# Performance work log

Hardware: AMD Instinct MI355X
Metric: run time of the kernel (lower is better)

## Reference

```python
import jax, jax.numpy as jnp
import numpy as np

N_RBF = 16
N_HIDDEN = 64
CUTOFF = 5.0
N_ATOMS = 4096


def setup_inputs() -> dict:
    key = jax.random.key(0)
    ks = jax.random.split(key, 7)
    # Scale positions so the 5.0 cutoff yields a sparse-ish neighbor graph.
    positions = jax.random.normal(ks[0], (N_ATOMS, 3), dtype=jnp.float32) * 10.0
    s1 = 1.0 / np.sqrt(N_RBF)
    s2 = 1.0 / np.sqrt(N_HIDDEN)
    W1 = jax.random.normal(ks[1], (N_RBF, N_HIDDEN), dtype=jnp.float32) * s1
    b1 = jax.random.normal(ks[2], (N_HIDDEN,), dtype=jnp.float32) * 0.01
    W2 = jax.random.normal(ks[3], (N_HIDDEN, N_HIDDEN), dtype=jnp.float32) * s2
    b2 = jax.random.normal(ks[4], (N_HIDDEN,), dtype=jnp.float32) * 0.01
    W3 = jax.random.normal(ks[5], (N_HIDDEN, 1), dtype=jnp.float32) * s2
    b3 = jax.random.normal(ks[6], (1,), dtype=jnp.float32) * 0.01
    return {"positions": positions, "W1": W1, "b1": b1, "W2": W2, "b2": b2, "W3": W3, "b3": b3}


def _features(positions):
    # positions: (N, 3) -> per-node RBF-aggregated features (N, n_rbf).
    # Equivalent to torch mask.nonzero + scatter_add: features[i] = sum_j in-cutoff rbf(d_ij).
    diff = positions[:, None, :] - positions[None, :, :]          # (N, N, 3)
    dist = jnp.sqrt(jnp.sum(diff * diff, axis=-1))                # (N, N)
    mask = (dist > 1e-6) & (dist < CUTOFF)                        # (N, N)
    centers = jnp.linspace(0.5, CUTOFF, N_RBF, dtype=jnp.float32) # (n_rbf,)
    eta = 0.5 * CUTOFF / N_RBF
    gauss = jnp.exp(-((dist[..., None] - centers) ** 2) / (2.0 * eta * eta))  # (N, N, n_rbf)
    x = jnp.minimum(dist / CUTOFF, 1.0)
    smooth = 0.5 * (1.0 + jnp.cos(jnp.float32(np.pi) * x))        # (N, N)
    w = jnp.where(mask, smooth, 0.0)                              # masked smooth-cutoff weight
    return jnp.einsum('ij,ijk->ik', w, gauss)                     # (N, n_rbf)


def reference(positions, W1, b1, W2, b2, W3, b3):
    feats = _features(positions)                                  # (N, n_rbf)
    h = jax.nn.silu(feats @ W1 + b1)
    h = jax.nn.silu(h @ W2 + b2)
    energy = jnp.sum(h @ W3 + b3)                                 # scalar
    return energy
```

## Files before the change

kernel.cpp:

```cpp
#include <hip/hip_runtime.h>

#define N_ATOMS  4096
#define N_RBF    16
#define N_HIDDEN 64
#define NTHREADS 1024
#define WPB      16
#define APB      8
#define NBLOCKS  (N_ATOMS / APB)
#define QCAP     192
#define HALF_J   (N_ATOMS / 2)

__global__ void zero_out_kernel(float* __restrict__ out) {
    if (threadIdx.x == 0 && blockIdx.x == 0) out[0] = 0.0f;
}

__device__ __forceinline__ void accum_rbf(float d2, float (&f)[N_RBF]) {
    const float d  = sqrtf(d2);
    const float sm = 0.5f + 0.5f * __cosf(0.62831853071795865f * d);
    #pragma unroll
    for (int k = 0; k < N_RBF; ++k) {
        const float t = d - (0.5f + 0.3f * (float)k);
        f[k] += sm * __expf(-20.48f * t * t);
    }
}

__device__ __forceinline__ int wave_prefix(unsigned long long m) {
    return __builtin_amdgcn_mbcnt_hi((unsigned)(m >> 32),
            __builtin_amdgcn_mbcnt_lo((unsigned)m, 0u));
}

__global__ __launch_bounds__(NTHREADS, 8) void fused_sr_kernel(
    const float* __restrict__ pos,
    const float* __restrict__ W1,
    const float* __restrict__ b1,
    const float* __restrict__ W2,
    const float* __restrict__ b2,
    const float* __restrict__ W3,
    const float* __restrict__ b3,
    float* __restrict__ out)
{
    __shared__ __align__(16) float4 sp[N_ATOMS];
    __shared__ __align__(16) float qd[WPB][QCAP];
    __shared__ float pairbuf[APB][2][N_RBF];
    __shared__ float ered[APB];

    const int tid = threadIdx.x;

    for (int idx = tid; idx < N_ATOMS; idx += NTHREADS) {
        sp[idx] = make_float4(pos[idx * 3 + 0], pos[idx * 3 + 1], pos[idx * 3 + 2], 0.0f);
    }
    __syncthreads();

    const int lane = tid & 63;
    const int wib  = tid >> 6;
    const int pid  = wib >> 1;
    const int half = wib & 1;
    const int i    = blockIdx.x * APB + pid;

    const float4 pi4 = sp[i];
    const float xi = pi4.x, yi = pi4.y, zi = pi4.z;

    int cnt = 0;
    const int jbase = half * HALF_J;
    #pragma unroll 4
    for (int j0 = 0; j0 < HALF_J; j0 += 64) {
        const float4 pj = sp[jbase + j0 + lane];
        const float dx = xi - pj.x;
        const float dy = yi - pj.y;
        const float dz = zi - pj.z;
        const float d2 = fmaf(dx, dx, fmaf(dy, dy, dz * dz));
        const bool act = (d2 < 25.0f) && (d2 > 1e-12f);
        const unsigned long long m = __ballot(act);
        int widx = cnt + wave_prefix(m);
        widx = widx < QCAP ? widx : QCAP - 1;
        if (act) qd[wib][widx] = d2;
        cnt += (int)__popcll(m);
    }

    float f[N_RBF];
    #pragma unroll
    for (int k = 0; k < N_RBF; ++k) f[k] = 0.0f;
    for (int b = 0; b < cnt; b += 64) {
        const int q = b + lane;
        accum_rbf((q < cnt) ? qd[wib][q] : 1e8f, f);
    }

    #pragma unroll
    for (int k = 0; k < N_RBF; ++k) {
        #pragma unroll
        for (int off = 32; off > 0; off >>= 1)
            f[k] += __shfl_xor(f[k], off, 64);
    }

    if (lane == 0) {
        #pragma unroll
        for (int k = 0; k < N_RBF; ++k) pairbuf[pid][half][k] = f[k];
    }
    __syncthreads();

    if (half == 0) {
        float a1 = b1[lane];
        #pragma unroll
        for (int k = 0; k < N_RBF; ++k)
            a1 = fmaf(f[k] + pairbuf[pid][1][k], W1[k * N_HIDDEN + lane], a1);
        const float h1 = a1 / (1.0f + __expf(-a1));

        float* h1p = &qd[pid][0];
        h1p[lane] = h1;
        float a2 = b2[lane];
        #pragma unroll
        for (int k = 0; k < N_HIDDEN; k += 4) {
            const float4 hv = *reinterpret_cast<const float4*>(&h1p[k]);
            a2 = fmaf(hv.x, W2[(k + 0) * N_HIDDEN + lane], a2);
            a2 = fmaf(hv.y, W2[(k + 1) * N_HIDDEN + lane], a2);
            a2 = fmaf(hv.z, W2[(k + 2) * N_HIDDEN + lane], a2);
            a2 = fmaf(hv.w, W2[(k + 3) * N_HIDDEN + lane], a2);
        }
        const float h2 = a2 / (1.0f + __expf(-a2));

        float e = h2 * W3[lane];
        #pragma unroll
        for (int off = 32; off > 0; off >>= 1)
            e += __shfl_xor(e, off, 64);
        if (lane == 0) ered[pid] = e;
    }
    __syncthreads();
    if (tid == 0) {
        float acc = 0.0f;
        #pragma unroll
        for (int w = 0; w < APB; ++w) acc += ered[w];
        atomicAdd(out, acc + (float)APB * b3[0]);
    }
}

extern "C" void kernel_launch(void* const* d_in, const int* in_sizes, int n_in,
                              void* d_out, int out_size, void* d_ws, size_t ws_size,
                              hipStream_t stream) {
    const float* pos = (const float*)d_in[0];
    const float* W1  = (const float*)d_in[1];
    const float* b1  = (const float*)d_in[2];
    const float* W2  = (const float*)d_in[3];
    const float* b2  = (const float*)d_in[4];
    const float* W3  = (const float*)d_in[5];
    const float* b3  = (const float*)d_in[6];
    float* out = (float*)d_out;

    zero_out_kernel<<<1, 64, 0, stream>>>(out);
    fused_sr_kernel<<<NBLOCKS, NTHREADS, 0, stream>>>(pos, W1, b1, W2, b2, W3, b3, out);
}
```

Measured before the change: 86.29 us.

## Process two atoms per wave in neighbor scan and rebalance RBF/MLP across waves

Each block now handles 16 atoms instead of 8, and each wave scans half the j range for two atoms at once, so every loaded neighbor position is reused for two distance tests. After the scan, the per-wave queues are regrouped so that each wave owns one atom. That wave runs the RBF accumulation and the MLP for its atom, using a shared-memory transpose to finish the feature reduction. This halves the number of blocks, and with it the redundant per-block copy of all 4096 positions into LDS. It also keeps every wave busy during the MLP instead of idling half of them, at the cost of an extra barrier and a different LDS footprint.

```diff
diff --git a/kernel.cpp b/kernel.cpp
--- a/kernel.cpp
+++ b/kernel.cpp
@@ -5,7 +5,7 @@
 #define N_HIDDEN 64
 #define NTHREADS 1024
 #define WPB      16
-#define APB      8
+#define APB      16
 #define NBLOCKS  (N_ATOMS / APB)
 #define QCAP     192
 #define HALF_J   (N_ATOMS / 2)
@@ -29,7 +29,7 @@
             __builtin_amdgcn_mbcnt_lo((unsigned)m, 0u));
 }
 
-__global__ __launch_bounds__(NTHREADS, 8) void fused_sr_kernel(
+__global__ __launch_bounds__(NTHREADS) void fused_sr_kernel(
     const float* __restrict__ pos,
     const float* __restrict__ W1,
     const float* __restrict__ b1,
@@ -40,9 +40,10 @@
     float* __restrict__ out)
 {
     __shared__ __align__(16) float4 sp[N_ATOMS];
-    __shared__ __align__(16) float qd[WPB][QCAP];
-    __shared__ float pairbuf[APB][2][N_RBF];
-    __shared__ float ered[APB];
+    __shared__ __align__(16) float  qd[APB][2][QCAP];
+    __shared__ int qcnt[APB][2];
+    __shared__ __align__(16) float  h1buf[WPB][N_HIDDEN];
+    __shared__ float ered[WPB];
 
     const int tid = threadIdx.x;
 
@@ -52,83 +53,113 @@
     __syncthreads();
 
     const int lane = tid & 63;
-    const int wib  = tid >> 6;
-    const int pid  = wib >> 1;
-    const int half = wib & 1;
-    const int i    = blockIdx.x * APB + pid;
+    const int w    = tid >> 6;
+    const int t    = w >> 1;
+    const int h    = w & 1;
+    const int iA   = blockIdx.x * APB + 2 * t;
 
-    const float4 pi4 = sp[i];
-    const float xi = pi4.x, yi = pi4.y, zi = pi4.z;
+    const float4 pa = sp[iA];
+    const float4 pb = sp[iA + 1];
+    const int jbase = h * HALF_J;
 
-    int cnt = 0;
-    const int jbase = half * HALF_J;
+    int cntA = 0, cntB = 0;
     #pragma unroll 4
     for (int j0 = 0; j0 < HALF_J; j0 += 64) {
         const float4 pj = sp[jbase + j0 + lane];
-        const float dx = xi - pj.x;
-        const float dy = yi - pj.y;
-        const float dz = zi - pj.z;
-        const float d2 = fmaf(dx, dx, fmaf(dy, dy, dz * dz));
-        const bool act = (d2 < 25.0f) && (d2 > 1e-12f);
-        const unsigned long long m = __ballot(act);
-        int widx = cnt + wave_prefix(m);
-        widx = widx < QCAP ? widx : QCAP - 1;
-        if (act) qd[wib][widx] = d2;
-        cnt += (int)__popcll(m);
+        {
+            const float dx = pa.x - pj.x, dy = pa.y - pj.y, dz = pa.z - pj.z;
+            const float d2 = fmaf(dx, dx, fmaf(dy, dy, dz * dz));
+            const bool act = (d2 < 25.0f) && (d2 > 1e-12f);
+            const unsigned long long m = __ballot(act);
+            int widx = cntA + wave_prefix(m);
+            widx = widx < QCAP ? widx : QCAP - 1;
+            if (act) qd[2 * t + 0][h][widx] = d2;
+            cntA += (int)__popcll(m);
+        }
+        {
+            const float dx = pb.x - pj.x, dy = pb.y - pj.y, dz = pb.z - pj.z;
+            const float d2 = fmaf(dx, dx, fmaf(dy, dy, dz * dz));
+            const bool act = (d2 < 25.0f) && (d2 > 1e-12f);
+            const unsigned long long m = __ballot(act);
+            int widx = cntB + wave_prefix(m);
+            widx = widx < QCAP ? widx : QCAP - 1;
+            if (act) qd[2 * t + 1][h][widx] = d2;
+            cntB += (int)__popcll(m);
+        }
     }
+    if (lane == 0) { qcnt[2 * t + 0][h] = cntA; qcnt[2 * t + 1][h] = cntB; }
+    __syncthreads();
+
+    const int aloc = 2 * t + h;
+    const int ia   = blockIdx.x * APB + aloc;
+    (void)ia;
 
     float f[N_RBF];
     #pragma unroll
     for (int k = 0; k < N_RBF; ++k) f[k] = 0.0f;
-    for (int b = 0; b < cnt; b += 64) {
-        const int q = b + lane;
-        accum_rbf((q < cnt) ? qd[wib][q] : 1e8f, f);
+    #pragma unroll
+    for (int part = 0; part < 2; ++part) {
+        const int c = qcnt[aloc][part];
+        for (int b = 0; b < c; b += 64) {
+            const int q = b + lane;
+            accum_rbf((q < c) ? qd[aloc][part][q] : 1e8f, f);
+        }
     }
 
     #pragma unroll
     for (int k = 0; k < N_RBF; ++k) {
+        f[k] += __shfl_xor(f[k], 32, 64);
+        f[k] += __shfl_xor(f[k], 16, 64);
+    }
+    float* tb = &qd[aloc][0][0];
+    if (lane < 16) {
         #pragma unroll
-        for (int off = 32; off > 0; off >>= 1)
-            f[k] += __shfl_xor(f[k], off, 64);
+        for (int j = 0; j < 16; j += 4)
+            *reinterpret_cast<float4*>(&tb[lane * 16 + j]) =
+                make_float4(f[j], f[j + 1], f[j + 2], f[j + 3]);
+    }
+    const int kk = lane & 15, rep = lane >> 4;
+    float F = 0.0f;
+    #pragma unroll
+    for (int i = 0; i < 4; ++i) F += tb[(4 * rep + i) * 16 + kk];
+    F += __shfl_xor(F, 16, 64);
+    F += __shfl_xor(F, 32, 64);
+    if (lane < 16) tb[256 + lane] = F;
+    float Fb[N_RBF];
+    #pragma unroll
+    for (int j = 0; j < 16; j += 4) {
+        const float4 v = *reinterpret_cast<const float4*>(&tb[256 + j]);
+        Fb[j] = v.x; Fb[j + 1] = v.y; Fb[j + 2] = v.z; Fb[j + 3] = v.w;
     }
 
-    if (lane == 0) {
-        #pragma unroll
-        for (int k = 0; k < N_RBF; ++k) pairbuf[pid][half][k] = f[k];
+    float a1 = b1[lane];
+    #pragma unroll
+    for (int k = 0; k < N_RBF; ++k)
+        a1 = fmaf(Fb[k], W1[k * N_HIDDEN + lane], a1);
+    const float h1 = a1 / (1.0f + __expf(-a1));
+
+    h1buf[w][lane] = h1;
+    float a2 = b2[lane];
+    #pragma unroll
+    for (int k = 0; k < N_HIDDEN; k += 4) {
+        const float4 hv = *reinterpret_cast<const float4*>(&h1buf[w][k]);
+        a2 = fmaf(hv.x, W2[(k + 0) * N_HIDDEN + lane], a2);
+        a2 = fmaf(hv.y, W2[(k + 1) * N_HIDDEN + lane], a2);
+        a2 = fmaf(hv.z, W2[(k + 2) * N_HIDDEN + lane], a2);
+        a2 = fmaf(hv.w, W2[(k + 3) * N_HIDDEN + lane], a2);
     }
-    __syncthreads();
+    const float h2 = a2 / (1.0f + __expf(-a2));
 
-    if (half == 0) {
-        float a1 = b1[lane];
-        #pragma unroll
-        for (int k = 0; k < N_RBF; ++k)
-            a1 = fmaf(f[k] + pairbuf[pid][1][k], W1[k * N_HIDDEN + lane], a1);
-        const float h1 = a1 / (1.0f + __expf(-a1));
-
-        float* h1p = &qd[pid][0];
-        h1p[lane] = h1;
-        float a2 = b2[lane];
-        #pragma unroll
-        for (int k = 0; k < N_HIDDEN; k += 4) {
-            const float4 hv = *reinterpret_cast<const float4*>(&h1p[k]);
-            a2 = fmaf(hv.x, W2[(k + 0) * N_HIDDEN + lane], a2);
-            a2 = fmaf(hv.y, W2[(k + 1) * N_HIDDEN + lane], a2);
-            a2 = fmaf(hv.z, W2[(k + 2) * N_HIDDEN + lane], a2);
-            a2 = fmaf(hv.w, W2[(k + 3) * N_HIDDEN + lane], a2);
-        }
-        const float h2 = a2 / (1.0f + __expf(-a2));
-
-        float e = h2 * W3[lane];
-        #pragma unroll
-        for (int off = 32; off > 0; off >>= 1)
-            e += __shfl_xor(e, off, 64);
-        if (lane == 0) ered[pid] = e;
-    }
+    float e = h2 * W3[lane];
+    #pragma unroll
+    for (int off = 32; off > 0; off >>= 1)
+        e += __shfl_xor(e, off, 64);
+    if (lane == 0) ered[w] = e;
     __syncthreads();
     if (tid == 0) {
         float acc = 0.0f;
         #pragma unroll
-        for (int w = 0; w < APB; ++w) acc += ered[w];
+        for (int v = 0; v < WPB; ++v) acc += ered[v];
         atomicAdd(out, acc + (float)APB * b3[0]);
     }
 }
```

Result: faster. 79.91 us (-7.4%).
